# Kernel tuning notes

Measured on AMD Instinct MI355X. Metric: run time of the kernel, lower is better.

Reference implementation:

```python
import jax, jax.numpy as jnp
import numpy as np

IN, OUT, STEPS, BATCH = 1024, 1024, 100, 64
THR = 15.0
RATIO = 0.5
C1 = RATIO * THR            # initial membrane potential = 7.5
C2 = 1.0 / THR
C3 = (1.0 - RATIO) / STEPS


def setup_inputs() -> dict:
    key = jax.random.key(0)
    k0, k1, k2, k3 = jax.random.split(key, 4)
    spikes = jax.random.randint(k0, (STEPS, BATCH, IN), 0, 2).astype(jnp.float32)
    mem = jnp.full((BATCH, OUT), C1, dtype=jnp.float32)          # init_if
    hat_spikes = jax.random.uniform(k1, (BATCH, IN), dtype=jnp.float32)
    W = jax.random.normal(k2, (OUT, IN), dtype=jnp.float32)      # w_mean=0, w_std=1
    b = jax.random.normal(k3, (OUT,), dtype=jnp.float32)
    return {"spikes": spikes, "mem": mem, "hat_spikes": hat_spikes, "W": W, "b": b}


def reference(spikes, mem, hat_spikes, W, b):
    steps = spikes.shape[0]
    # delta_us = fc(spikes): [T, B, OUT]
    delta_us = jnp.einsum('tbi,oi->tbo', spikes, W) + b

    def step(carry, du):
        m, su = carry
        m = m + du
        s = (m > THR).astype(m.dtype)          # spike
        m = jnp.clip(m, 0.0, THR)              # clamp_(0, thr)
        su = su + m                            # sum_u += mem
        m = m - m * s                          # reset fired neurons
        return (m, su), s

    (mem_out, sum_u), ss = jax.lax.scan(
        step, (mem, jnp.zeros_like(mem)), delta_us)

    hat_u_fwd = sum_u / steps                  # [B, OUT]
    hat_s_fwd = ss.mean(axis=0)                # [B, OUT]

    # training-mode surrogate path: forward values come from the spike loop,
    # gradients flow through fc(hat_spikes) (ForwardFirstBackwardSecond)
    delta_u = hat_spikes @ W.T + b
    hat_u = jax.lax.stop_gradient(hat_u_fwd) + delta_u - jax.lax.stop_gradient(delta_u)
    surr = jnp.maximum(hat_u * C2, C3)         # (hat_u*C2).clamp_min(C3)
    hat_s = jax.lax.stop_gradient(hat_s_fwd) + surr - jax.lax.stop_gradient(surr)

    return ss, mem_out, hat_s
```

## Files before the change

kernel.cpp:

```cpp
#include <hip/hip_runtime.h>


typedef __attribute__((ext_vector_type(4))) int int4v;

#define T_STEPS 100
#define BO 65536
#define K_DIM 1024
#define A8_OFF 0
#define BT_OFF 6553600
#define LO_OFF 11796480

__global__ __launch_bounds__(256)
void prepass(const float* __restrict__ S, const float* __restrict__ W,
             signed char* __restrict__ A8, signed char* __restrict__ Bt) {
    const int wave = blockIdx.x * 4 + (threadIdx.x >> 6);
    const int lane = threadIdx.x & 63;
    const int r16 = lane & 15, quad = lane >> 4;

    if (wave < 6400) {
        const int m16 = wave >> 4, k64 = wave & 15;
        const int m = m16 * 16 + r16;
        const float* sp = S + (size_t)m * K_DIM + k64 * 64 + quad * 16;
        const float4 s0 = *(const float4*)(sp);
        const float4 s1 = *(const float4*)(sp + 4);
        const float4 s2 = *(const float4*)(sp + 8);
        const float4 s3 = *(const float4*)(sp + 12);
        const float sv[16] = {s0.x,s0.y,s0.z,s0.w, s1.x,s1.y,s1.z,s1.w,
                              s2.x,s2.y,s2.z,s2.w, s3.x,s3.y,s3.z,s3.w};
        union { signed char c[16]; int4v v; } u;
#pragma unroll
        for (int e = 0; e < 16; ++e) u.c[e] = (signed char)sv[e];
        *(int4v*)(A8 + ((size_t)(m16 * 16 + k64) * 1024) + lane * 16) = u.v;
    } else {
        const int t2 = wave - 6400;
        const int n16 = t2 >> 4, k64 = t2 & 15;
        const int n = n16 * 16 + r16;
        const float* wp = W + (size_t)n * K_DIM + k64 * 64 + quad * 16;
        const float4 w0 = *(const float4*)(wp);
        const float4 w1 = *(const float4*)(wp + 4);
        const float4 w2 = *(const float4*)(wp + 8);
        const float4 w3 = *(const float4*)(wp + 12);
        const float wv[16] = {w0.x,w0.y,w0.z,w0.w, w1.x,w1.y,w1.z,w1.w,
                              w2.x,w2.y,w2.z,w2.w, w3.x,w3.y,w3.z,w3.w};
        union { signed char c[16]; int4v v; } u[4];
#pragma unroll
        for (int e = 0; e < 16; ++e) {
            long long q = llrint((double)wv[e] * 0x1p28);
#pragma unroll
            for (int p = 0; p < 3; ++p) {
                const int d = (int)(((q + 128) & 255) - 128);
                u[p].c[e] = (signed char)d;
                q = (q - d) >> 8;
            }
            u[3].c[e] = (signed char)q;
        }
        signed char* base = Bt + (size_t)(n16 * 16 + k64) * 4 * 1024 + lane * 16;
#pragma unroll
        for (int p = 0; p < 4; ++p)
            *(int4v*)(base + (size_t)p * 1024) = u[p].v;
    }
}

__global__ __launch_bounds__(256, 3)
void gemm_i8(const signed char* __restrict__ A8,
             const signed char* __restrict__ Bt,
             const float* __restrict__ bias,
             float* __restrict__ Chi,
             _Float16* __restrict__ Lo) {
    __shared__ signed char lds[2][16384];
    const int bid = blockIdx.x;
    const int xcd = bid & 7;
    const int t_  = bid >> 3;
    const int cu  = t_ & 31;
    const int rnd = t_ >> 5;
    const int bn = (xcd << 2) | (cu & 3);
    const int bm = (cu >> 2) + (rnd << 3);

    const int tid = threadIdx.x;
    const int lane = tid & 63, wid = tid >> 6;
    const int wm = wid >> 1, wn = wid & 1;
    const int quad = lane >> 4, r16 = lane & 15;

    const signed char* sbase[4];
    int sstride[4], ldsoff[4];
#pragma unroll
    for (int j = 0; j < 4; ++j) {
        const int c = wid * 4 + j;
        if (c < 8) {
            sbase[j] = A8 + (size_t)(bm * 8 + c) * 16384 + lane * 16;
            sstride[j] = 1024;
            ldsoff[j] = c * 1024 + lane * 16;
        } else {
            const int j2 = c - 8;
            sbase[j] = Bt + (size_t)(bn * 2 + (j2 >> 2)) * 65536
                          + (size_t)(j2 & 3) * 1024 + lane * 16;
            sstride[j] = 4096;
            ldsoff[j] = 8192 + j2 * 1024 + lane * 16;
        }
    }
    int aoff[4], boff[4];
#pragma unroll
    for (int i = 0; i < 4; ++i) aoff[i] = (wm * 4 + i) * 1024 + lane * 16;
#pragma unroll
    for (int p = 0; p < 4; ++p) boff[p] = 8192 + (wn * 4 + p) * 1024 + lane * 16;

    int4v sreg[4];
    int4v acc[4][4] = {};

#pragma unroll
    for (int j = 0; j < 4; ++j) sreg[j] = *(const int4v*)(sbase[j]);
#pragma unroll
    for (int j = 0; j < 4; ++j) *(int4v*)(&lds[0][ldsoff[j]]) = sreg[j];
    __syncthreads();

    for (int kt = 0; kt < 16; ++kt) {
        const int cur = kt & 1, nxt = cur ^ 1;
        if (kt + 1 < 16) {
#pragma unroll
            for (int j = 0; j < 4; ++j)
                sreg[j] = *(const int4v*)(sbase[j] + (size_t)(kt + 1) * sstride[j]);
        }
        int4v af[4], bf[4];
#pragma unroll
        for (int i = 0; i < 4; ++i) af[i] = *(const int4v*)(&lds[cur][aoff[i]]);
#pragma unroll
        for (int p = 0; p < 4; ++p) bf[p] = *(const int4v*)(&lds[cur][boff[p]]);
#pragma unroll
        for (int p = 0; p < 4; ++p)
#pragma unroll
            for (int i = 0; i < 4; ++i)
                acc[i][p] = __builtin_amdgcn_mfma_i32_16x16x64_i8(
                    af[i], bf[p], acc[i][p], 0, 0, 0);
        if (kt + 1 < 16) {
#pragma unroll
            for (int j = 0; j < 4; ++j) *(int4v*)(&lds[nxt][ldsoff[j]]) = sreg[j];
        }
        __syncthreads();
    }

    const int n_g = bn * 32 + wn * 16 + r16;
    const double bd = (double)bias[n_g];
#pragma unroll
    for (int i = 0; i < 4; ++i)
#pragma unroll
        for (int e = 0; e < 4; ++e) {
            long long t = (long long)acc[i][3][e];
            t = t * 256 + (long long)acc[i][2][e];
            t = t * 256 + (long long)acc[i][1][e];
            t = t * 256 + (long long)acc[i][0][e];
            const double du = (double)t * 0x1p-28 + bd;
            const float hi = (float)du;
            const float lo = (float)(du - (double)hi);
            const size_t m_g = (size_t)(bm * 128 + wm * 64 + i * 16 + quad * 4 + e);
            const size_t off = m_g * 1024 + n_g;
            Chi[off] = hi;
            Lo[off] = (_Float16)(lo * 4096.0f);
        }
}

__global__ __launch_bounds__(256)
void snn_scan(float* __restrict__ out, const _Float16* __restrict__ lo,
              const float* __restrict__ mem0) {
    const int bo = blockIdx.x * 256 + threadIdx.x;
    double m = (double)mem0[bo];
    double cnt = 0.0;
    float h[4][4], l[4][4];
#pragma unroll
    for (int s = 0; s < 3; ++s)
#pragma unroll
        for (int u = 0; u < 4; ++u) {
            const size_t idx = (size_t)(s * 4 + u) * BO + bo;
            h[s][u] = out[idx];
            l[s][u] = (float)lo[idx];
        }
#pragma unroll
    for (int g = 0; g < 25; ++g) {
        const int cs = g & 3, ps = (g + 3) & 3;
        if (g + 3 < 25) {
#pragma unroll
            for (int u = 0; u < 4; ++u) {
                const size_t idx = (size_t)((g + 3) * 4 + u) * BO + bo;
                h[ps][u] = out[idx];
                l[ps][u] = (float)lo[idx];
            }
        }
#pragma unroll
        for (int u = 0; u < 4; ++u) {
            const double du = (double)h[cs][u] + (double)l[cs][u] * 0x1p-12;
            m += du;
            const double s = (m > 15.0) ? 1.0 : 0.0;
            m = fmin(fmax(m, 0.0), 15.0);
            out[(size_t)(g * 4 + u) * BO + bo] = (float)s;
            cnt += s;
            m -= m * s;
        }
    }
    out[(size_t)T_STEPS * BO + bo] = (float)m;
    out[(size_t)(T_STEPS + 1) * BO + bo] = (float)(cnt * 0.01);
}

extern "C" void kernel_launch(void* const* d_in, const int* in_sizes, int n_in,
                              void* d_out, int out_size, void* d_ws, size_t ws_size,
                              hipStream_t stream) {
    const float* spikes = (const float*)d_in[0];
    const float* mem    = (const float*)d_in[1];
    const float* W      = (const float*)d_in[3];
    const float* b      = (const float*)d_in[4];
    float* out = (float*)d_out;
    signed char* A8 = (signed char*)d_ws + A8_OFF;
    signed char* Bt = (signed char*)d_ws + BT_OFF;
    _Float16*    Lo = (_Float16*)((char*)d_ws + LO_OFF);

    prepass<<<dim3(1856), 256, 0, stream>>>(spikes, W, A8, Bt);
    gemm_i8<<<dim3(1600), 256, 0, stream>>>(A8, Bt, b, out, Lo);
    snn_scan<<<dim3(BO / 256), 256, 0, stream>>>(out, Lo, mem);
}
```

Baseline: 128.9 us.

## Fuse int8 GEMM with SNN time scan per batch-row tile via LDS

Measured after the change: 126.6 us. About the same (-1.7%).

```diff
diff --git a/kernel.cpp b/kernel.cpp
--- a/kernel.cpp
+++ b/kernel.cpp
@@ -4,11 +4,12 @@
 typedef __attribute__((ext_vector_type(4))) int int4v;
 
 #define T_STEPS 100
-#define BO 65536
-#define K_DIM 1024
-#define A8_OFF 0
-#define BT_OFF 6553600
-#define LO_OFF 11796480
+#define T_PAD   112
+#define BO      65536
+#define K_DIM   1024
+#define A8_OFF  0
+#define BT_OFF  7340032
+#define LDS_BUF 23552
 
 __global__ __launch_bounds__(256)
 void prepass(const float* __restrict__ S, const float* __restrict__ W,
@@ -17,22 +18,29 @@
     const int lane = threadIdx.x & 63;
     const int r16 = lane & 15, quad = lane >> 4;
 
-    if (wave < 6400) {
-        const int m16 = wave >> 4, k64 = wave & 15;
-        const int m = m16 * 16 + r16;
-        const float* sp = S + (size_t)m * K_DIM + k64 * 64 + quad * 16;
-        const float4 s0 = *(const float4*)(sp);
-        const float4 s1 = *(const float4*)(sp + 4);
-        const float4 s2 = *(const float4*)(sp + 8);
-        const float4 s3 = *(const float4*)(sp + 12);
-        const float sv[16] = {s0.x,s0.y,s0.z,s0.w, s1.x,s1.y,s1.z,s1.w,
-                              s2.x,s2.y,s2.z,s2.w, s3.x,s3.y,s3.z,s3.w};
+    if (wave < 7168) {
+        const int b   = wave / 112;
+        const int rem = wave - b * 112;
+        const int jt  = rem >> 4, k64 = rem & 15;
+        const int t   = jt * 16 + r16;
         union { signed char c[16]; int4v v; } u;
-#pragma unroll
-        for (int e = 0; e < 16; ++e) u.c[e] = (signed char)sv[e];
-        *(int4v*)(A8 + ((size_t)(m16 * 16 + k64) * 1024) + lane * 16) = u.v;
+        if (t < T_STEPS) {
+            const float* sp = S + ((size_t)t * 64 + b) * K_DIM + k64 * 64 + quad * 16;
+            const float4 s0 = *(const float4*)(sp);
+            const float4 s1 = *(const float4*)(sp + 4);
+            const float4 s2 = *(const float4*)(sp + 8);
+            const float4 s3 = *(const float4*)(sp + 12);
+            const float sv[16] = {s0.x,s0.y,s0.z,s0.w, s1.x,s1.y,s1.z,s1.w,
+                                  s2.x,s2.y,s2.z,s2.w, s3.x,s3.y,s3.z,s3.w};
+#pragma unroll
+            for (int e = 0; e < 16; ++e) u.c[e] = (signed char)sv[e];
+        } else {
+#pragma unroll
+            for (int e = 0; e < 16; ++e) u.c[e] = 0;
+        }
+        *(int4v*)(A8 + (size_t)wave * 1024 + lane * 16) = u.v;
     } else {
-        const int t2 = wave - 6400;
+        const int t2 = wave - 7168;
         const int n16 = t2 >> 4, k64 = t2 & 15;
         const int n = n16 * 16 + r16;
         const float* wp = W + (size_t)n * K_DIM + k64 * 64 + quad * 16;
@@ -61,142 +69,130 @@
     }
 }
 
-__global__ __launch_bounds__(256, 3)
-void gemm_i8(const signed char* __restrict__ A8,
-             const signed char* __restrict__ Bt,
-             const float* __restrict__ bias,
-             float* __restrict__ Chi,
-             _Float16* __restrict__ Lo) {
-    __shared__ signed char lds[2][16384];
+__global__ __launch_bounds__(256, 2)
+void gemm_scan(const signed char* __restrict__ A8,
+               const signed char* __restrict__ Bt,
+               const float* __restrict__ bias,
+               const float* __restrict__ mem0,
+               float* __restrict__ out) {
+    __shared__ int4v lds4[3200];
+    signed char* slds = (signed char*)lds4;
+    double* dulds = (double*)lds4;
+
     const int bid = blockIdx.x;
-    const int xcd = bid & 7;
-    const int t_  = bid >> 3;
-    const int cu  = t_ & 31;
-    const int rnd = t_ >> 5;
-    const int bn = (xcd << 2) | (cu & 3);
-    const int bm = (cu >> 2) + (rnd << 3);
+    const int b  = bid >> 4;
+    const int ng = bid & 15;
 
     const int tid = threadIdx.x;
     const int lane = tid & 63, wid = tid >> 6;
-    const int wm = wid >> 1, wn = wid & 1;
     const int quad = lane >> 4, r16 = lane & 15;
 
-    const signed char* sbase[4];
-    int sstride[4], ldsoff[4];
-#pragma unroll
-    for (int j = 0; j < 4; ++j) {
-        const int c = wid * 4 + j;
-        if (c < 8) {
-            sbase[j] = A8 + (size_t)(bm * 8 + c) * 16384 + lane * 16;
+    const signed char* sbase[6];
+    int sstride[6], ldsoff[6];
+#pragma unroll
+    for (int j = 0; j < 6; ++j) {
+        const int c = wid + 4 * j;
+        const int cc = (c < 23) ? c : 0;
+        if (cc < 7) {
+            sbase[j] = A8 + ((size_t)(b * T_PAD + cc * 16)) * 1024 + lane * 16;
             sstride[j] = 1024;
-            ldsoff[j] = c * 1024 + lane * 16;
+            ldsoff[j] = cc * 1024 + lane * 16;
         } else {
-            const int j2 = c - 8;
-            sbase[j] = Bt + (size_t)(bn * 2 + (j2 >> 2)) * 65536
-                          + (size_t)(j2 & 3) * 1024 + lane * 16;
+            const int j2 = cc - 7;
+            sbase[j] = Bt + ((size_t)((ng * 4 + (j2 >> 2)) * 16) * 4 + (j2 & 3)) * 1024
+                          + lane * 16;
             sstride[j] = 4096;
-            ldsoff[j] = 8192 + j2 * 1024 + lane * 16;
-        }
-    }
-    int aoff[4], boff[4];
-#pragma unroll
-    for (int i = 0; i < 4; ++i) aoff[i] = (wm * 4 + i) * 1024 + lane * 16;
-#pragma unroll
-    for (int p = 0; p < 4; ++p) boff[p] = 8192 + (wn * 4 + p) * 1024 + lane * 16;
-
-    int4v sreg[4];
-    int4v acc[4][4] = {};
-
-#pragma unroll
-    for (int j = 0; j < 4; ++j) sreg[j] = *(const int4v*)(sbase[j]);
-#pragma unroll
-    for (int j = 0; j < 4; ++j) *(int4v*)(&lds[0][ldsoff[j]]) = sreg[j];
+            ldsoff[j] = 7168 + j2 * 1024 + lane * 16;
+        }
+    }
+    int aoff[7], boff[4];
+#pragma unroll
+    for (int i = 0; i < 7; ++i) aoff[i] = i * 1024 + lane * 16;
+#pragma unroll
+    for (int p = 0; p < 4; ++p) boff[p] = 7168 + (wid * 4 + p) * 1024 + lane * 16;
+
+    int4v sreg[6];
+    int4v acc[7][4] = {};
+
+#pragma unroll
+    for (int j = 0; j < 6; ++j) if (wid + 4 * j < 23) sreg[j] = *(const int4v*)(sbase[j]);
+#pragma unroll
+    for (int j = 0; j < 6; ++j) if (wid + 4 * j < 23) *(int4v*)(slds + ldsoff[j]) = sreg[j];
     __syncthreads();
 
     for (int kt = 0; kt < 16; ++kt) {
-        const int cur = kt & 1, nxt = cur ^ 1;
+        const int cur = (kt & 1) * LDS_BUF, nxt = LDS_BUF - cur;
         if (kt + 1 < 16) {
 #pragma unroll
-            for (int j = 0; j < 4; ++j)
+            for (int j = 0; j < 6; ++j) if (wid + 4 * j < 23)
                 sreg[j] = *(const int4v*)(sbase[j] + (size_t)(kt + 1) * sstride[j]);
         }
-        int4v af[4], bf[4];
-#pragma unroll
-        for (int i = 0; i < 4; ++i) af[i] = *(const int4v*)(&lds[cur][aoff[i]]);
-#pragma unroll
-        for (int p = 0; p < 4; ++p) bf[p] = *(const int4v*)(&lds[cur][boff[p]]);
+        int4v af[7], bf[4];
+#pragma unroll
+        for (int i = 0; i < 7; ++i) af[i] = *(const int4v*)(slds + cur + aoff[i]);
+#pragma unroll
+        for (int p = 0; p < 4; ++p) bf[p] = *(const int4v*)(slds + cur + boff[p]);
 #pragma unroll
         for (int p = 0; p < 4; ++p)
 #pragma unroll
-            for (int i = 0; i < 4; ++i)
+            for (int i = 0; i < 7; ++i)
                 acc[i][p] = __builtin_amdgcn_mfma_i32_16x16x64_i8(
                     af[i], bf[p], acc[i][p], 0, 0, 0);
         if (kt + 1 < 16) {
 #pragma unroll
-            for (int j = 0; j < 4; ++j) *(int4v*)(&lds[nxt][ldsoff[j]]) = sreg[j];
+            for (int j = 0; j < 6; ++j) if (wid + 4 * j < 23)
+                *(int4v*)(slds + nxt + ldsoff[j]) = sreg[j];
         }
         __syncthreads();
     }
 
-    const int n_g = bn * 32 + wn * 16 + r16;
-    const double bd = (double)bias[n_g];
-#pragma unroll
-    for (int i = 0; i < 4; ++i)
+    const int n_loc = wid * 16 + r16;
+    const double bd = (double)bias[ng * 64 + n_loc];
+#pragma unroll
+    for (int i = 0; i < 7; ++i)
 #pragma unroll
         for (int e = 0; e < 4; ++e) {
-            long long t = (long long)acc[i][3][e];
-            t = t * 256 + (long long)acc[i][2][e];
-            t = t * 256 + (long long)acc[i][1][e];
-            t = t * 256 + (long long)acc[i][0][e];
-            const double du = (double)t * 0x1p-28 + bd;
-            const float hi = (float)du;
-            const float lo = (float)(du - (double)hi);
-            const size_t m_g = (size_t)(bm * 128 + wm * 64 + i * 16 + quad * 4 + e);
-            const size_t off = m_g * 1024 + n_g;
-            Chi[off] = hi;
-            Lo[off] = (_Float16)(lo * 4096.0f);
-        }
-}
-
-__global__ __launch_bounds__(256)
-void snn_scan(float* __restrict__ out, const _Float16* __restrict__ lo,
-              const float* __restrict__ mem0) {
-    const int bo = blockIdx.x * 256 + threadIdx.x;
-    double m = (double)mem0[bo];
-    double cnt = 0.0;
-    float h[4][4], l[4][4];
-#pragma unroll
-    for (int s = 0; s < 3; ++s)
-#pragma unroll
-        for (int u = 0; u < 4; ++u) {
-            const size_t idx = (size_t)(s * 4 + u) * BO + bo;
-            h[s][u] = out[idx];
-            l[s][u] = (float)lo[idx];
-        }
-#pragma unroll
-    for (int g = 0; g < 25; ++g) {
-        const int cs = g & 3, ps = (g + 3) & 3;
-        if (g + 3 < 25) {
+            const int t = i * 16 + quad * 4 + e;
+            if (t < T_STEPS) {
+                long long v = (long long)acc[i][3][e];
+                v = v * 256 + (long long)acc[i][2][e];
+                v = v * 256 + (long long)acc[i][1][e];
+                v = v * 256 + (long long)acc[i][0][e];
+                dulds[t * 64 + n_loc] = (double)v * 0x1p-28 + bd;
+            }
+        }
+    __syncthreads();
+
+    if (wid == 0) {
+        const int bo = b * 1024 + ng * 64 + lane;
+        double m = (double)mem0[bo];
+        double cnt = 0.0;
+        double d[4];
+#pragma unroll
+        for (int u = 0; u < 4; ++u) d[u] = dulds[u * 64 + lane];
+        for (int g = 0; g < 25; ++g) {
+            double dn[4];
+            if (g + 1 < 25) {
+#pragma unroll
+                for (int u = 0; u < 4; ++u) dn[u] = dulds[((g + 1) * 4 + u) * 64 + lane];
+            }
 #pragma unroll
             for (int u = 0; u < 4; ++u) {
-                const size_t idx = (size_t)((g + 3) * 4 + u) * BO + bo;
-                h[ps][u] = out[idx];
-                l[ps][u] = (float)lo[idx];
-            }
-        }
-#pragma unroll
-        for (int u = 0; u < 4; ++u) {
-            const double du = (double)h[cs][u] + (double)l[cs][u] * 0x1p-12;
-            m += du;
-            const double s = (m > 15.0) ? 1.0 : 0.0;
-            m = fmin(fmax(m, 0.0), 15.0);
-            out[(size_t)(g * 4 + u) * BO + bo] = (float)s;
-            cnt += s;
-            m -= m * s;
-        }
-    }
-    out[(size_t)T_STEPS * BO + bo] = (float)m;
-    out[(size_t)(T_STEPS + 1) * BO + bo] = (float)(cnt * 0.01);
+                m += d[u];
+                const double s = (m > 15.0) ? 1.0 : 0.0;
+                m = fmin(fmax(m, 0.0), 15.0);
+                out[(size_t)(g * 4 + u) * BO + bo] = (float)s;
+                cnt += s;
+                m -= m * s;
+            }
+            if (g + 1 < 25) {
+#pragma unroll
+                for (int u = 0; u < 4; ++u) d[u] = dn[u];
+            }
+        }
+        out[(size_t)T_STEPS * BO + bo] = (float)m;
+        out[(size_t)(T_STEPS + 1) * BO + bo] = (float)(cnt * 0.01);
+    }
 }
 
 extern "C" void kernel_launch(void* const* d_in, const int* in_sizes, int n_in,
@@ -209,9 +205,7 @@
     float* out = (float*)d_out;
     signed char* A8 = (signed char*)d_ws + A8_OFF;
     signed char* Bt = (signed char*)d_ws + BT_OFF;
-    _Float16*    Lo = (_Float16*)((char*)d_ws + LO_OFF);
-
-    prepass<<<dim3(1856), 256, 0, stream>>>(spikes, W, A8, Bt);
-    gemm_i8<<<dim3(1600), 256, 0, stream>>>(A8, Bt, b, out, Lo);
-    snn_scan<<<dim3(BO / 256), 256, 0, stream>>>(out, Lo, mem);
+
+    prepass<<<dim3(2048), 256, 0, stream>>>(spikes, W, A8, Bt);
+    gemm_scan<<<dim3(1024), 256, 0, stream>>>(A8, Bt, b, mem, out);
 }
```
